# Optimization experiments

Hardware: AMD Instinct MI355X
Metric: run time of the kernel (lower is better)

## Reference

```python
import jax, jax.numpy as jnp
import numpy as np

N = 50000
E = 800000
D = 128
EPS = 1e-12  # torch F.normalize eps


def setup_inputs() -> dict:
    key = jax.random.key(0)
    ks = jax.random.split(key, 8)
    x = jax.random.normal(ks[0], (N, D), dtype=jnp.float32)
    edge_index = jax.random.randint(ks[1], (2, E), 0, N, dtype=jnp.int64)
    s = 1.0 / np.sqrt(D)
    # project MLP (Linear(D, D) + bias, followed by relu in SAGEConv)
    Wp = jax.random.uniform(ks[2], (D, D), jnp.float32, -s, s)
    bp = jax.random.uniform(ks[3], (D,), jnp.float32, -s, s)
    # lin_l: applied to aggregated neighbor features (with bias)
    Wl = jax.random.uniform(ks[4], (D, D), jnp.float32, -s, s)
    bl = jax.random.uniform(ks[5], (D,), jnp.float32, -s, s)
    # lin_r: applied to root features (no bias)
    Wr = jax.random.uniform(ks[6], (D, D), jnp.float32, -s, s)
    return {"x": x, "edge_index": edge_index, "Wp": Wp, "bp": bp,
            "Wl": Wl, "bl": bl, "Wr": Wr}


def reference(x, edge_index, Wp, bp, Wl, bl, Wr):
    src, dst = edge_index[0], edge_index[1]
    n = x.shape[0]
    # project=True: per-node projection + relu (applied before gather, same math)
    h = jax.nn.relu(x @ Wp.T + bp)                      # [N, D]
    # gather messages from source nodes, mean-aggregate at targets
    msg = h[src]                                        # [E, D]
    agg = jax.ops.segment_sum(msg, dst, num_segments=n)  # [N, D]
    cnt = jax.ops.segment_sum(jnp.ones((msg.shape[0],), x.dtype), dst,
                              num_segments=n)
    mean = agg / jnp.maximum(cnt, 1.0)[:, None]         # nodes w/o edges -> 0
    # combine: lin_l(agg) + lin_r(x)
    out = mean @ Wl.T + bl + x @ Wr.T                   # [N, D]
    # elementwise tail: ELU -> (dropout p=0, eval) -> L2 normalize -> residual
    out = jax.nn.elu(out)
    norm = jnp.sqrt(jnp.sum(out * out, axis=-1, keepdims=True))
    out = out / jnp.maximum(norm, EPS)
    return x + out
```

## Files before the change

### kernel.cpp

```cpp
#include <hip/hip_runtime.h>
#include <hip/hip_bf16.h>

#define DD 128
#define EPSN 1e-12f
#define MAXDEG 64
#define EPB_A 4096
#define EPB_B 2048

typedef __attribute__((ext_vector_type(8))) short bf16x8;
typedef __attribute__((ext_vector_type(4))) float f32x4;

__device__ __forceinline__ short bfbits(float f) {
  unsigned u = __float_as_uint(f);
  u += 0x7FFF + ((u >> 16) & 1);
  return (short)(u >> 16);
}
__device__ __forceinline__ float bf2f(short s) {
  return __uint_as_float(((unsigned)(unsigned short)s) << 16);
}
__device__ __forceinline__ unsigned packbf(float a, float b) {
  return (unsigned)(unsigned short)bfbits(a) |
         ((unsigned)(unsigned short)bfbits(b) << 16);
}

__global__ __launch_bounds__(512) void k_projA(
    const float* __restrict__ x, const float* __restrict__ Wp,
    const float* __restrict__ bp, unsigned short* __restrict__ h,
    const int* __restrict__ ei, unsigned* __restrict__ seg,
    int* __restrict__ cnt8, int* __restrict__ cnt,
    int n, int nE, int nABlk, unsigned scale, int segCap)
{
  __shared__ uint4 WuP[2048];
  int b = blockIdx.x;
  int tid = threadIdx.x;

  if (b < nABlk) {
    int* bcnt = (int*)&WuP[0];
    int* bcur = bcnt + 8;
    if (tid < 8) bcnt[tid] = 0;
    int zi = b * 256 + tid;
    if (tid < 256 && zi < n) cnt[zi] = 0;
    __syncthreads();
    int base = b * EPB_A;
    int dv[8], sv[8], bv[8];
    bool val[8];
#pragma unroll
    for (int u = 0; u < 8; ++u) {
      int e = base + u * 512 + tid;
      val[u] = (e < nE);
      if (val[u]) {
        dv[u] = ei[nE + e];
        sv[u] = ei[e];
        bv[u] = (int)(((unsigned long long)(unsigned)dv[u] * scale) >> 32);
        atomicAdd(&bcnt[bv[u]], 1);
      }
    }
    __syncthreads();
    if (tid < 8) bcur[tid] = atomicAdd(&cnt8[tid], bcnt[tid]);
    __syncthreads();
#pragma unroll
    for (int u = 0; u < 8; ++u) {
      if (val[u]) {
        int pos = atomicAdd(&bcur[bv[u]], 1);
        if (pos < segCap)
          seg[(size_t)bv[u] * segCap + pos] =
              ((unsigned)dv[u] << 16) | (unsigned)sv[u];
      }
    }
    return;
  }

#pragma unroll
  for (int it = 0; it < 4; ++it) {
    int g = it * 512 + tid;
    int row = g >> 4, j = g & 15;
    const float* src = Wp + row * DD + j * 8;
    float4 f0 = *(const float4*)src;
    float4 f1 = *(const float4*)(src + 4);
    uint4 v;
    v.x = packbf(f0.x, f0.y); v.y = packbf(f0.z, f0.w);
    v.z = packbf(f1.x, f1.y); v.w = packbf(f1.z, f1.w);
    WuP[(row << 4) | (j ^ (row & 15))] = v;
  }
  __syncthreads();

  int l = tid & 63;
  int wv = tid >> 6;
  int row0 = ((b - nABlk) * 8 + wv) * 16;
  if (row0 >= n) return;
  int lr = l & 15, kg = l >> 4;
  int rA = row0 + lr; if (rA > n - 1) rA = n - 1;

  f32x4 acc[8];
#pragma unroll
  for (int cb = 0; cb < 8; ++cb) {
    float bv2 = bp[16 * cb + lr];
    acc[cb] = (f32x4){bv2, bv2, bv2, bv2};
  }

  const float* xrow = x + (size_t)rA * DD;
#pragma unroll
  for (int ks = 0; ks < 4; ++ks) {
    int ko = 32 * ks + 8 * kg;
    float4 f0 = *(const float4*)(xrow + ko);
    float4 f1 = *(const float4*)(xrow + ko + 4);
    float fv[8] = {f0.x, f0.y, f0.z, f0.w, f1.x, f1.y, f1.z, f1.w};
    bf16x8 ah, al;
#pragma unroll
    for (int j = 0; j < 8; ++j) {
      short hb = bfbits(fv[j]);
      ah[j] = hb;
      al[j] = bfbits(fv[j] - bf2f(hb));
    }
    int ju = 4 * ks + kg;
#pragma unroll
    for (int cb = 0; cb < 8; ++cb) {
      int row = 16 * cb + lr;
      bf16x8 bfr = *(const bf16x8*)&WuP[(row << 4) | (ju ^ lr)];
      acc[cb] = __builtin_amdgcn_mfma_f32_16x16x32_bf16(ah, bfr, acc[cb], 0, 0, 0);
      acc[cb] = __builtin_amdgcn_mfma_f32_16x16x32_bf16(al, bfr, acc[cb], 0, 0, 0);
    }
  }

#pragma unroll
  for (int i = 0; i < 4; ++i) {
    int r = row0 + 4 * kg + i;
    if (r < n) {
#pragma unroll
      for (int cb = 0; cb < 8; ++cb) {
        float v = fmaxf(acc[cb][i], 0.f);
        h[(size_t)r * DD + 16 * cb + lr] = (unsigned short)bfbits(v);
      }
    }
  }
}

__global__ __launch_bounds__(256) void k_passB(
    const unsigned* __restrict__ seg, const int* __restrict__ cnt8,
    int* __restrict__ cnt, unsigned short* __restrict__ slots, int segCap)
{
  int b = blockIdx.x;
  int tid = threadIdx.x;
  int r = b & 7;
  int chunk = b >> 3;
  int len = cnt8[r]; if (len > segCap) len = segCap;
  const unsigned* s = seg + (size_t)r * segCap;
  int base = chunk * EPB_B;
#pragma unroll
  for (int u = 0; u < 8; ++u) {
    int e = base + u * 256 + tid;
    if (e < len) {
      unsigned p = s[e];
      int d = (int)(p >> 16);
      int src = (int)(p & 0xFFFFu);
      int pos = atomicAdd(&cnt[d], 1);
      if (pos < MAXDEG) slots[(size_t)d * MAXDEG + pos] = (unsigned short)src;
    }
  }
}

__global__ __launch_bounds__(256) void k_gather(
    const int* __restrict__ cnt, const unsigned short* __restrict__ slots,
    const __hip_bfloat162* __restrict__ h2,
    __hip_bfloat162* __restrict__ meanb, int n)
{
  int w = (blockIdx.x * 256 + threadIdx.x) >> 6;
  int l = threadIdx.x & 63;
  int node0 = w * 4;
  if (node0 >= n) return;

#pragma unroll 1
  for (int i = 0; i < 4; ++i) {
    int node = node0 + i;
    if (node >= n) break;
    int dgTrue = cnt[node];
    int dg = dgTrue < MAXDEG ? dgTrue : MAXDEG;
    int myidx = (int)slots[(size_t)node * MAXDEG + l];

    float s0 = 0.f, s1 = 0.f, t0 = 0.f, t1 = 0.f;
    int j = 0;
    for (; j + 8 <= dg; j += 8) {
      int i0 = __builtin_amdgcn_readlane(myidx, j);
      int i1 = __builtin_amdgcn_readlane(myidx, j + 1);
      int i2 = __builtin_amdgcn_readlane(myidx, j + 2);
      int i3 = __builtin_amdgcn_readlane(myidx, j + 3);
      int i4 = __builtin_amdgcn_readlane(myidx, j + 4);
      int i5 = __builtin_amdgcn_readlane(myidx, j + 5);
      int i6 = __builtin_amdgcn_readlane(myidx, j + 6);
      int i7 = __builtin_amdgcn_readlane(myidx, j + 7);
      __hip_bfloat162 v0 = h2[(size_t)i0 * 64 + l];
      __hip_bfloat162 v1 = h2[(size_t)i1 * 64 + l];
      __hip_bfloat162 v2 = h2[(size_t)i2 * 64 + l];
      __hip_bfloat162 v3 = h2[(size_t)i3 * 64 + l];
      __hip_bfloat162 v4 = h2[(size_t)i4 * 64 + l];
      __hip_bfloat162 v5 = h2[(size_t)i5 * 64 + l];
      __hip_bfloat162 v6 = h2[(size_t)i6 * 64 + l];
      __hip_bfloat162 v7 = h2[(size_t)i7 * 64 + l];
      s0 += __bfloat162float(v0.x) + __bfloat162float(v1.x);
      s1 += __bfloat162float(v0.y) + __bfloat162float(v1.y);
      t0 += __bfloat162float(v2.x) + __bfloat162float(v3.x);
      t1 += __bfloat162float(v2.y) + __bfloat162float(v3.y);
      s0 += __bfloat162float(v4.x) + __bfloat162float(v5.x);
      s1 += __bfloat162float(v4.y) + __bfloat162float(v5.y);
      t0 += __bfloat162float(v6.x) + __bfloat162float(v7.x);
      t1 += __bfloat162float(v6.y) + __bfloat162float(v7.y);
    }
    for (; j < dg; ++j) {
      int i0 = __builtin_amdgcn_readlane(myidx, j);
      __hip_bfloat162 v0 = h2[(size_t)i0 * 64 + l];
      s0 += __bfloat162float(v0.x);
      s1 += __bfloat162float(v0.y);
    }
    s0 += t0; s1 += t1;
    float rd = 1.0f / fmaxf((float)dgTrue, 1.0f);
    __hip_bfloat162 o;
    o.x = __float2bfloat16(s0 * rd);
    o.y = __float2bfloat16(s1 * rd);
    meanb[(size_t)node * 64 + l] = o;
  }
}

__global__ __launch_bounds__(512) void k_combine(
    const float* __restrict__ x, const float* __restrict__ Wl,
    const float* __restrict__ bl, const float* __restrict__ Wr,
    const unsigned short* __restrict__ meanb,
    float* __restrict__ out, int n)
{
  __shared__ uint4 Wu[4096];
  __shared__ float ssh[4 * 32];

  int tid = threadIdx.x;

#pragma unroll
  for (int it = 0; it < 8; ++it) {
    int g = it * 512 + tid;
    int mat = g >> 11, rem = g & 2047;
    int row = rem >> 4, j = rem & 15;
    const float* src = (mat ? Wr : Wl) + row * DD + j * 8;
    float4 f0 = *(const float4*)src;
    float4 f1 = *(const float4*)(src + 4);
    uint4 v;
    v.x = packbf(f0.x, f0.y); v.y = packbf(f0.z, f0.w);
    v.z = packbf(f1.x, f1.y); v.w = packbf(f1.z, f1.w);
    Wu[(mat << 11) | (row << 4) | (j ^ (row & 15))] = v;
  }
  __syncthreads();

  int l = tid & 63;
  int wv = tid >> 6;
  int rg = wv >> 1;
  int half = wv & 1;
  int row0 = (blockIdx.x * 4 + rg) * 16;
  int lr = l & 15, kg = l >> 4;
  bool active = (row0 < n);

  f32x4 acc[4];
  float ss[4] = {0.f, 0.f, 0.f, 0.f};

  if (active) {
    int rA = row0 + lr; if (rA > n - 1) rA = n - 1;
#pragma unroll
    for (int q = 0; q < 4; ++q) {
      float bv = bl[16 * (4 * half + q) + lr];
      acc[q] = (f32x4){bv, bv, bv, bv};
    }

    const unsigned short* mrow = meanb + (size_t)rA * DD;
    const float* xrow = x + (size_t)rA * DD;
#pragma unroll
    for (int ks = 0; ks < 4; ++ks) {
      int ko = 32 * ks + 8 * kg;
      bf16x8 a = *(const bf16x8*)(mrow + ko);
      float4 f0 = *(const float4*)(xrow + ko);
      float4 f1 = *(const float4*)(xrow + ko + 4);
      float fv[8] = {f0.x, f0.y, f0.z, f0.w, f1.x, f1.y, f1.z, f1.w};
      bf16x8 ah, al;
#pragma unroll
      for (int jj = 0; jj < 8; ++jj) {
        short hb = bfbits(fv[jj]);
        ah[jj] = hb;
        al[jj] = bfbits(fv[jj] - bf2f(hb));
      }
      int ju = 4 * ks + kg;
#pragma unroll
      for (int q = 0; q < 4; ++q) {
        int row = 16 * (4 * half + q) + lr;
        bf16x8 bL = *(const bf16x8*)&Wu[(0 << 11) | (row << 4) | (ju ^ lr)];
        bf16x8 bR = *(const bf16x8*)&Wu[(1 << 11) | (row << 4) | (ju ^ lr)];
        acc[q] = __builtin_amdgcn_mfma_f32_16x16x32_bf16(a,  bL, acc[q], 0, 0, 0);
        acc[q] = __builtin_amdgcn_mfma_f32_16x16x32_bf16(ah, bR, acc[q], 0, 0, 0);
        acc[q] = __builtin_amdgcn_mfma_f32_16x16x32_bf16(al, bR, acc[q], 0, 0, 0);
      }
    }

#pragma unroll
    for (int q = 0; q < 4; ++q) {
#pragma unroll
      for (int i = 0; i < 4; ++i) {
        float z = acc[q][i];
        z = z > 0.f ? z : expm1f(z);
        acc[q][i] = z;
        ss[i] += z * z;
      }
    }
#pragma unroll
    for (int i = 0; i < 4; ++i) {
#pragma unroll
      for (int m2 = 1; m2 < 16; m2 <<= 1) ss[i] += __shfl_xor(ss[i], m2);
    }
    if (lr == 0) {
#pragma unroll
      for (int i = 0; i < 4; ++i) ssh[rg * 32 + half * 16 + 4 * kg + i] = ss[i];
    }
  }
  __syncthreads();

  if (active) {
#pragma unroll
    for (int i = 0; i < 4; ++i) {
      int r = row0 + 4 * kg + i;
      if (r < n) {
        float tot = ssh[rg * 32 + 4 * kg + i] + ssh[rg * 32 + 16 + 4 * kg + i];
        float inv = 1.f / fmaxf(sqrtf(tot), EPSN);
#pragma unroll
        for (int q = 0; q < 4; ++q) {
          int c = 16 * (4 * half + q) + lr;
          out[(size_t)r * DD + c] = x[(size_t)r * DD + c] + acc[q][i] * inv;
        }
      }
    }
  }
}

extern "C" void kernel_launch(void* const* d_in, const int* in_sizes, int n_in,
                              void* d_out, int out_size, void* d_ws, size_t ws_size,
                              hipStream_t stream) {
  const float* x  = (const float*)d_in[0];
  const int*   ei = (const int*)d_in[1];
  const float* Wp = (const float*)d_in[2];
  const float* bp = (const float*)d_in[3];
  const float* Wl = (const float*)d_in[4];
  const float* bl = (const float*)d_in[5];
  const float* Wr = (const float*)d_in[6];
  float* out = (float*)d_out;

  int n  = in_sizes[0] / DD;
  int nE = in_sizes[1] / 2;
  int segCap = nE / 8 + 16384;
  unsigned scale = (unsigned)((((unsigned long long)8) << 32) / (unsigned long long)n);

  auto align256 = [](size_t v) { return (v + 255) & ~(size_t)255; };
  char* p = (char*)d_ws;
  unsigned short* h = (unsigned short*)p;      p += align256((size_t)n * DD * 2);
  unsigned short* meanb = (unsigned short*)p;  p += align256((size_t)n * DD * 2);
  int* cnt  = (int*)p;                         p += align256((size_t)n * 4);
  int* cnt8 = (int*)p;                         p += 256;
  unsigned short* slots = (unsigned short*)p;  p += align256((size_t)n * MAXDEG * 2);
  unsigned* seg = (unsigned*)p;                p += align256((size_t)8 * segCap * 4);

  hipMemsetAsync(cnt8, 0, 256, stream);

  int nABlk = (nE + EPB_A - 1) / EPB_A;
  int nPBlk = (n + 127) / 128;
  k_projA<<<nABlk + nPBlk, 512, 0, stream>>>(
      x, Wp, bp, h, ei, seg, cnt8, cnt, n, nE, nABlk, scale, segCap);

  int nChunkB = (segCap + EPB_B - 1) / EPB_B;
  k_passB<<<8 * nChunkB, 256, 0, stream>>>(seg, cnt8, cnt, slots, segCap);

  int nGWaves = (n + 3) / 4;
  int nGBlk   = (nGWaves + 3) / 4;
  k_gather<<<nGBlk, 256, 0, stream>>>(
      cnt, slots, (const __hip_bfloat162*)h, (__hip_bfloat162*)meanb, n);

  int nCBlk = (n + 63) / 64;
  k_combine<<<nCBlk, 512, 0, stream>>>(x, Wl, bl, Wr, meanb, out, n);
}
```

Before: 112.9 us.

## Bin edges by destination into fine bins and build slot lists in LDS inside gather

Partitions edges into roughly 98 bins of 512 destination nodes instead of 8 coarse bins. The separate global-atomic pass that scattered sources into per-node slot arrays is removed. Each gather block now scans its bin's segment, builds per-node slot lists in shared memory with LDS atomics, and then aggregates. This drops one kernel launch, the global cnt and slots traffic, and the global atomics. In exchange each bin's segment is read four times, once by each of the four 128-node blocks covering it, and the fixed segment capacity per bin is tighter, which risks dropping edges when a bin overflows.

```diff
diff --git a/kernel.cpp b/kernel.cpp
--- a/kernel.cpp
+++ b/kernel.cpp
@@ -5,7 +5,8 @@
 #define EPSN 1e-12f
 #define MAXDEG 64
 #define EPB_A 4096
-#define EPB_B 2048
+#define BIN_SHIFT 9
+#define NPB 128
 
 typedef __attribute__((ext_vector_type(8))) short bf16x8;
 typedef __attribute__((ext_vector_type(4))) float f32x4;
@@ -27,8 +28,8 @@
     const float* __restrict__ x, const float* __restrict__ Wp,
     const float* __restrict__ bp, unsigned short* __restrict__ h,
     const int* __restrict__ ei, unsigned* __restrict__ seg,
-    int* __restrict__ cnt8, int* __restrict__ cnt,
-    int n, int nE, int nABlk, unsigned scale, int segCap)
+    int* __restrict__ binCnt, int n, int nE, int nABlk,
+    int nBins, int segCap)
 {
   __shared__ uint4 WuP[2048];
   int b = blockIdx.x;
@@ -36,10 +37,8 @@
 
   if (b < nABlk) {
     int* bcnt = (int*)&WuP[0];
-    int* bcur = bcnt + 8;
-    if (tid < 8) bcnt[tid] = 0;
-    int zi = b * 256 + tid;
-    if (tid < 256 && zi < n) cnt[zi] = 0;
+    int* bcur = bcnt + nBins;
+    if (tid < nBins) bcnt[tid] = 0;
     __syncthreads();
     int base = b * EPB_A;
     int dv[8], sv[8], bv[8];
@@ -51,12 +50,12 @@
       if (val[u]) {
         dv[u] = ei[nE + e];
         sv[u] = ei[e];
-        bv[u] = (int)(((unsigned long long)(unsigned)dv[u] * scale) >> 32);
+        bv[u] = dv[u] >> BIN_SHIFT;
         atomicAdd(&bcnt[bv[u]], 1);
       }
     }
     __syncthreads();
-    if (tid < 8) bcur[tid] = atomicAdd(&cnt8[tid], bcnt[tid]);
+    if (tid < nBins) bcur[tid] = atomicAdd(&binCnt[tid], bcnt[tid]);
     __syncthreads();
 #pragma unroll
     for (int u = 0; u < 8; ++u) {
@@ -135,47 +134,43 @@
   }
 }
 
-__global__ __launch_bounds__(256) void k_passB(
-    const unsigned* __restrict__ seg, const int* __restrict__ cnt8,
-    int* __restrict__ cnt, unsigned short* __restrict__ slots, int segCap)
+__global__ __launch_bounds__(256) void k_gath2(
+    const unsigned* __restrict__ seg, const int* __restrict__ binCnt,
+    const __hip_bfloat162* __restrict__ h2,
+    __hip_bfloat162* __restrict__ meanb, int n, int segCap)
 {
+  __shared__ int lcnt[NPB];
+  __shared__ unsigned short lslot[NPB * MAXDEG];
   int b = blockIdx.x;
   int tid = threadIdx.x;
-  int r = b & 7;
-  int chunk = b >> 3;
-  int len = cnt8[r]; if (len > segCap) len = segCap;
-  const unsigned* s = seg + (size_t)r * segCap;
-  int base = chunk * EPB_B;
-#pragma unroll
-  for (int u = 0; u < 8; ++u) {
-    int e = base + u * 256 + tid;
-    if (e < len) {
-      unsigned p = s[e];
-      int d = (int)(p >> 16);
-      int src = (int)(p & 0xFFFFu);
-      int pos = atomicAdd(&cnt[d], 1);
-      if (pos < MAXDEG) slots[(size_t)d * MAXDEG + pos] = (unsigned short)src;
-    }
-  }
-}
-
-__global__ __launch_bounds__(256) void k_gather(
-    const int* __restrict__ cnt, const unsigned short* __restrict__ slots,
-    const __hip_bfloat162* __restrict__ h2,
-    __hip_bfloat162* __restrict__ meanb, int n)
-{
-  int w = (blockIdx.x * 256 + threadIdx.x) >> 6;
-  int l = threadIdx.x & 63;
-  int node0 = w * 4;
-  if (node0 >= n) return;
-
+  int lo = b * NPB;
+  int bin = lo >> BIN_SHIFT;
+
+  if (tid < NPB) lcnt[tid] = 0;
+  __syncthreads();
+
+  int len = binCnt[bin]; if (len > segCap) len = segCap;
+  const unsigned* s = seg + (size_t)bin * segCap;
+  for (int e = tid; e < len; e += 256) {
+    unsigned p = s[e];
+    int dl = (int)(p >> 16) - lo;
+    if ((unsigned)dl < NPB) {
+      int pos = atomicAdd(&lcnt[dl], 1);
+      if (pos < MAXDEG) lslot[dl * MAXDEG + pos] = (unsigned short)(p & 0xFFFFu);
+    }
+  }
+  __syncthreads();
+
+  int l = tid & 63;
+  int wv = tid >> 6;
 #pragma unroll 1
-  for (int i = 0; i < 4; ++i) {
-    int node = node0 + i;
+  for (int i = 0; i < 32; ++i) {
+    int dl = wv * 32 + i;
+    int node = lo + dl;
     if (node >= n) break;
-    int dgTrue = cnt[node];
+    int dgTrue = lcnt[dl];
     int dg = dgTrue < MAXDEG ? dgTrue : MAXDEG;
-    int myidx = (int)slots[(size_t)node * MAXDEG + l];
+    int myidx = (int)lslot[dl * MAXDEG + l];
 
     float s0 = 0.f, s1 = 0.f, t0 = 0.f, t1 = 0.f;
     int j = 0;
@@ -346,32 +341,26 @@
 
   int n  = in_sizes[0] / DD;
   int nE = in_sizes[1] / 2;
-  int segCap = nE / 8 + 16384;
-  unsigned scale = (unsigned)((((unsigned long long)8) << 32) / (unsigned long long)n);
+  int nBins = (n + 511) >> BIN_SHIFT;
+  int segCap = nE / nBins + 2048;
 
   auto align256 = [](size_t v) { return (v + 255) & ~(size_t)255; };
   char* p = (char*)d_ws;
   unsigned short* h = (unsigned short*)p;      p += align256((size_t)n * DD * 2);
   unsigned short* meanb = (unsigned short*)p;  p += align256((size_t)n * DD * 2);
-  int* cnt  = (int*)p;                         p += align256((size_t)n * 4);
-  int* cnt8 = (int*)p;                         p += 256;
-  unsigned short* slots = (unsigned short*)p;  p += align256((size_t)n * MAXDEG * 2);
-  unsigned* seg = (unsigned*)p;                p += align256((size_t)8 * segCap * 4);
-
-  hipMemsetAsync(cnt8, 0, 256, stream);
+  int* binCnt = (int*)p;                       p += align256((size_t)nBins * 4);
+  unsigned* seg = (unsigned*)p;                p += align256((size_t)nBins * segCap * 4);
+
+  hipMemsetAsync(binCnt, 0, (size_t)nBins * 4, stream);
 
   int nABlk = (nE + EPB_A - 1) / EPB_A;
   int nPBlk = (n + 127) / 128;
   k_projA<<<nABlk + nPBlk, 512, 0, stream>>>(
-      x, Wp, bp, h, ei, seg, cnt8, cnt, n, nE, nABlk, scale, segCap);
-
-  int nChunkB = (segCap + EPB_B - 1) / EPB_B;
-  k_passB<<<8 * nChunkB, 256, 0, stream>>>(seg, cnt8, cnt, slots, segCap);
-
-  int nGWaves = (n + 3) / 4;
-  int nGBlk   = (nGWaves + 3) / 4;
-  k_gather<<<nGBlk, 256, 0, stream>>>(
-      cnt, slots, (const __hip_bfloat162*)h, (__hip_bfloat162*)meanb, n);
+      x, Wp, bp, h, ei, seg, binCnt, n, nE, nABlk, nBins, segCap);
+
+  int nGBlk = (n + NPB - 1) / NPB;
+  k_gath2<<<nGBlk, 256, 0, stream>>>(
+      seg, binCnt, (const __hip_bfloat162*)h, (__hip_bfloat162*)meanb, n, segCap);
 
   int nCBlk = (n + 63) / 64;
   k_combine<<<nCBlk, 512, 0, stream>>>(x, Wl, bl, Wr, meanb, out, n);
```

After: 137.4 us. +21.8%, slower.
